# Kernel tuning notes

Hardware: AMD Instinct MI355X
Metric: run time of the kernel (lower is better)

## Reference

```python
import jax, jax.numpy as jnp
import numpy as np

GRAPH_ALPHA = 3.0
HOP_ALPHA = 0.05
TOP_K = 30


def conv1x1(x, W, b):
    # x: [B,C,N,T], W: [O,C] -> [B,O,N,T]
    return jnp.einsum('bcnt,oc->bont', x, W) + b[None, :, None, None]


def tconv(x, W, b):
    # temporal conv along T, kernel (1,3), 'same' padding. W: [O,I,1,3]
    y = jax.lax.conv_general_dilated(x, W, (1, 1), ((0, 0), (1, 1)),
                                     dimension_numbers=('NCHW', 'OIHW', 'NCHW'))
    return y + b[None, :, None, None]


def mixprop(x, adj, W, b):
    # 1-hop mix-prop graph diffusion (gcn_depth=1, hopalpha=0.05)
    n = adj.shape[0]
    A = adj + jnp.eye(n, dtype=adj.dtype)
    A = A / A.sum(axis=1, keepdims=True)
    h = HOP_ALPHA * x + (1.0 - HOP_ALPHA) * jnp.einsum('bcvt,vw->bcwt', x, A)
    return conv1x1(jnp.concatenate([x, h], axis=1), W, b)


def st_block(x, adj, tf_w, tf_b, tg_w, tg_b, g1_w, g1_b, g2_w, g2_b,
             end_w, end_b, out_w, out_b):
    h = jnp.tanh(tconv(x, tf_w, tf_b)) * jax.nn.sigmoid(tconv(x, tg_w, tg_b))
    h = mixprop(h, adj, g1_w, g1_b) + mixprop(h, adj.T, g2_w, g2_b)
    h = jax.nn.relu(conv1x1(h, end_w, end_b))
    return conv1x1(h, out_w, out_b)


def build_adj(idx, emb1, emb2, l1_w, l1_b, l2_w, l2_b):
    e1, e2 = emb1[idx], emb2[idx]
    n1 = jnp.tanh(GRAPH_ALPHA * (e1 @ l1_w.T + l1_b))
    n2 = jnp.tanh(GRAPH_ALPHA * (e2 @ l2_w.T + l2_b))
    a = n1 @ n2.T - n2 @ n1.T
    adj = jax.nn.relu(jnp.tanh(GRAPH_ALPHA * a))
    _, top_idx = jax.lax.top_k(adj, TOP_K)
    rows = jnp.arange(adj.shape[0])[:, None]
    mask = jnp.zeros_like(adj).at[rows, top_idx].set(1.0)
    return adj * mask


def setup_inputs() -> dict:
    B, T, N, D = 16, 128, 1024, 64
    ks = jax.random.split(jax.random.key(0), 24)
    def w(i, shape):
        return jax.random.normal(ks[i], shape, dtype=jnp.float32) * 0.1
    z = lambda *s: jnp.zeros(s, jnp.float32)
    return {
        'x': jax.random.normal(ks[0], (B, T, N), dtype=jnp.float32),
        'idx': jnp.arange(N, dtype=jnp.int32),
        'emb1': w(1, (N, D)), 'emb2': w(2, (N, D)),
        'lin1_w': w(3, (D, D)), 'lin1_b': z(D),
        'lin2_w': w(4, (D, D)), 'lin2_b': z(D),
        'w_start': w(5, (16, 1)), 'b_start': z(16),
        'enc_tf_w': w(6, (16, 16, 1, 3)), 'enc_tf_b': z(16),
        'enc_tg_w': w(7, (16, 16, 1, 3)), 'enc_tg_b': z(16),
        'enc_g1_w': w(8, (16, 32)), 'enc_g1_b': z(16),
        'enc_g2_w': w(9, (16, 32)), 'enc_g2_b': z(16),
        'enc_end_w': w(10, (32, 16)), 'enc_end_b': z(32),
        'enc_out_w': w(11, (64, 32)), 'enc_out_b': z(64),
        'dec_tf_w': w(12, (64, 64, 1, 3)), 'dec_tf_b': z(64),
        'dec_tg_w': w(13, (64, 64, 1, 3)), 'dec_tg_b': z(64),
        'dec_g1_w': w(14, (64, 128)), 'dec_g1_b': z(64),
        'dec_g2_w': w(15, (64, 128)), 'dec_g2_b': z(64),
        'dec_end_w': w(16, (32, 64)), 'dec_end_b': z(32),
        'dec_out_w': w(17, (16, 32)), 'dec_out_b': z(16),
        'w_end': w(18, (1, 16)), 'b_end': z(1),
    }


def reference(x, idx, emb1, emb2, lin1_w, lin1_b, lin2_w, lin2_b,
              w_start, b_start,
              enc_tf_w, enc_tf_b, enc_tg_w, enc_tg_b, enc_g1_w, enc_g1_b,
              enc_g2_w, enc_g2_b, enc_end_w, enc_end_b, enc_out_w, enc_out_b,
              dec_tf_w, dec_tf_b, dec_tg_w, dec_tg_b, dec_g1_w, dec_g1_b,
              dec_g2_w, dec_g2_b, dec_end_w, dec_end_b, dec_out_w, dec_out_b,
              w_end, b_end):
    adj = build_adj(idx, emb1, emb2, lin1_w, lin1_b, lin2_w, lin2_b)
    h = jnp.transpose(x, (0, 2, 1))[:, None]  # [B,1,N,T]
    h = conv1x1(h, w_start, b_start)          # [B,16,N,T]
    z = st_block(h, adj, enc_tf_w, enc_tf_b, enc_tg_w, enc_tg_b,
                 enc_g1_w, enc_g1_b, enc_g2_w, enc_g2_b,
                 enc_end_w, enc_end_b, enc_out_w, enc_out_b)  # [B,64,N,T]
    y = st_block(z, adj, dec_tf_w, dec_tf_b, dec_tg_w, dec_tg_b,
                 dec_g1_w, dec_g1_b, dec_g2_w, dec_g2_b,
                 dec_end_w, dec_end_b, dec_out_w, dec_out_b)  # [B,16,N,T]
    y = conv1x1(y, w_end, b_end)               # [B,1,N,T]
    return jnp.transpose(y[:, 0], (0, 2, 1))   # [B,T,N]
```

## Files before the change

kernel.cpp:

```cpp
#include <hip/hip_runtime.h>
#include <math.h>

#define NN   1024
#define TTL  128
#define NTP  131072
#define TOPK 30

#define OEGTF_T 0
#define OEGTF_C 48
#define OEGTF_B 96
#define OEGTG_T 112
#define OEGTG_C 160
#define OEGTG_B 208
#define OEE0    224
#define OEE1    736
#define OEE2    1248
#define OEEB    1760
#define OEOUT_W 1792
#define OEOUT_B 3840
#define ODTF_B  16192
#define ODTG_B  28544
#define ODEB    34752
#define OWC     34784
#define OBC     34816
#define ODEALL  59456
#define ODTW2   65600
#define OCF     77888
#define OCG     78080
#define WTOT    78272


__global__ void k_prep_weights(
    const float* __restrict__ w_start, const float* __restrict__ b_start,
    const float* __restrict__ etf_w, const float* __restrict__ etf_b,
    const float* __restrict__ etg_w, const float* __restrict__ etg_b,
    const float* __restrict__ eg1_w, const float* __restrict__ eg1_b,
    const float* __restrict__ eg2_w, const float* __restrict__ eg2_b,
    const float* __restrict__ eend_w, const float* __restrict__ eend_b,
    const float* __restrict__ eout_w, const float* __restrict__ eout_b,
    const float* __restrict__ dtf_w, const float* __restrict__ dtf_b,
    const float* __restrict__ dtg_w, const float* __restrict__ dtg_b,
    const float* __restrict__ dg1_w, const float* __restrict__ dg1_b,
    const float* __restrict__ dg2_w, const float* __restrict__ dg2_b,
    const float* __restrict__ dend_w, const float* __restrict__ dend_b,
    const float* __restrict__ dout_w, const float* __restrict__ dout_b,
    const float* __restrict__ w_end, const float* __restrict__ b_end,
    float* __restrict__ W)
{
    int tid = blockIdx.x*blockDim.x + threadIdx.x;
    int nthr = gridDim.x*blockDim.x;
    for (int id=tid; id<96; id+=nthr){
        int which = id/48; int r = id%48; int o = r/3, k = r%3;
        const float* w = which ? etg_w : etf_w;
        double t=0.0, c=0.0;
        for (int i=0;i<16;i++){
            double wv = (double)w[(o*16+i)*3+k];
            t += wv*(double)w_start[i];
            c += wv*(double)b_start[i];
        }
        W[(which?OEGTG_T:OEGTF_T)+o*3+k] = (float)t;
        W[(which?OEGTG_C:OEGTF_C)+o*3+k] = (float)c;
    }
    for (int i=tid;i<16;i+=nthr){
        W[OEGTF_B+i] = etf_b[i];
        W[OEGTG_B+i] = etg_b[i];
    }
    for (int id=tid; id<512; id+=nthr){
        int i = id>>5, o2 = id&31;
        double s0=0.0, s1=0.0, s2=0.0;
        for (int o=0;o<16;o++){
            double m0 = (double)eg1_w[o*32+i] + (double)eg2_w[o*32+i]
                      + 0.05*((double)eg1_w[o*32+16+i] + (double)eg2_w[o*32+16+i]);
            double m1 = 0.95*(double)eg1_w[o*32+16+i];
            double m2 = 0.95*(double)eg2_w[o*32+16+i];
            double ew = (double)eend_w[o2*16+o];
            s0 += ew*m0; s1 += ew*m1; s2 += ew*m2;
        }
        W[OEE0+i*32+o2]=(float)s0; W[OEE1+i*32+o2]=(float)s1; W[OEE2+i*32+o2]=(float)s2;
    }
    for (int o2=tid; o2<32; o2+=nthr){
        double s = (double)eend_b[o2];
        for (int o=0;o<16;o++) s += (double)eend_w[o2*16+o]*((double)eg1_b[o]+(double)eg2_b[o]);
        W[OEEB+o2] = (float)s;
    }
    for (int i=tid;i<64;i+=nthr){
        W[ODTF_B+i]=dtf_b[i]; W[ODTG_B+i]=dtg_b[i];
    }
    for (int id=tid; id<12288; id+=nthr){
        int oc = id/3072; int rem = id%3072; int j = rem/96; int q = rem%96;
        const float* w = (q<48) ? dtf_w : dtg_w;
        int q2 = (q<48) ? q : q-48;
        int o = q2/3, k = q2%3;
        double s = 0.0;
        for (int i=0;i<64;i++)
            s += (double)w[((oc*16+o)*64+i)*3+k]*(double)eout_w[i*32+j];
        W[ODTW2+id] = (float)s;
    }
    for (int id=tid; id<384; id+=nthr){
        int which = id/192; int r = id%192;
        int oc = r/48; int q = r%48; int o = q/3, k = q%3;
        const float* w = which ? dtg_w : dtf_w;
        double s = 0.0;
        for (int i=0;i<64;i++)
            s += (double)w[((oc*16+o)*64+i)*3+k]*(double)eout_b[i];
        W[(which?OCG:OCF) + oc*48 + o*3 + k] = (float)s;
    }
    for (int id=tid; id<6144; id+=nthr){
        int i = id/96, j = id%96;
        double s = 0.0;
        if (j < 32){
            int o2 = j;
            for (int o=0;o<64;o++){
                double m1 = 0.95*(double)dg1_w[o*128+64+i];
                s += (double)dend_w[o2*64+o]*m1;
            }
        } else if (j < 64){
            int o2 = j-32;
            for (int o=0;o<64;o++){
                double m2 = 0.95*(double)dg2_w[o*128+64+i];
                s += (double)dend_w[o2*64+o]*m2;
            }
        } else {
            int o2 = j-64;
            for (int o=0;o<64;o++){
                double m0 = (double)dg1_w[o*128+i] + (double)dg2_w[o*128+i]
                          + 0.05*((double)dg1_w[o*128+64+i] + (double)dg2_w[o*128+64+i]);
                s += (double)dend_w[o2*64+o]*m0;
            }
        }
        W[ODEALL+id] = (float)s;
    }
    for (int o2=tid; o2<32; o2+=nthr){
        double s = (double)dend_b[o2];
        for (int o=0;o<64;o++) s += (double)dend_w[o2*64+o]*((double)dg1_b[o]+(double)dg2_b[o]);
        W[ODEB+o2] = (float)s;
        double wc = 0.0;
        for (int o3=0;o3<16;o3++) wc += (double)w_end[o3]*(double)dout_w[o3*32+o2];
        W[OWC+o2] = (float)wc;
    }
    if (tid==0){
        double bc = (double)b_end[0];
        for (int o3=0;o3<16;o3++) bc += (double)w_end[o3]*(double)dout_b[o3];
        W[OBC] = (float)bc;
    }
}

__global__ void k_emb(const int* __restrict__ idxp,
                      const float* __restrict__ emb1, const float* __restrict__ emb2,
                      const float* __restrict__ l1w, const float* __restrict__ l1b,
                      const float* __restrict__ l2w, const float* __restrict__ l2b,
                      double* __restrict__ n1, double* __restrict__ n2)
{
    int id = blockIdx.x*blockDim.x + threadIdx.x;
    int i = id>>6, d = id&63;
    int ii = idxp[i];
    double a1 = (double)l1b[d], a2 = (double)l2b[d];
    for (int k=0;k<64;k++){
        a1 += (double)emb1[ii*64+k]*(double)l1w[d*64+k];
        a2 += (double)emb2[ii*64+k]*(double)l2w[d*64+k];
    }
    n1[id] = tanh(3.0*a1);
    n2[id] = tanh(3.0*a2);
}

__global__ __launch_bounds__(256) void k_topk(
    const double* __restrict__ n1, const double* __restrict__ n2,
    int* __restrict__ topc, double* __restrict__ topv,
    double* __restrict__ rs1, double* __restrict__ colsum)
{
    __shared__ double arow[NN];
    __shared__ double sn1[64], sn2[64];
    __shared__ double rvs[4];
    __shared__ int    rjs[4];
    int i = blockIdx.x, tid = threadIdx.x;
    int lane = tid & 63, wid = tid >> 6;
    if (tid < 64){ sn1[tid] = n1[i*64+tid]; sn2[tid] = n2[i*64+tid]; }
    __syncthreads();
    for (int jb=0;jb<4;jb++){
        int j = jb*256 + tid;
        const double* p2 = n2 + (long)j*64;
        const double* p1 = n1 + (long)j*64;
        double d1v=0.0, d2v=0.0;
        for (int d=0;d<64;d++){ d1v += sn1[d]*p2[d]; d2v += sn2[d]*p1[d]; }
        double a = tanh(3.0*(d1v - d2v));
        arow[j] = a>0.0 ? a : 0.0;
    }
    __syncthreads();
    double rsum = 0.0;
    for (int r=0;r<TOPK;r++){
        double bv = -2.0; int bj = 1<<30;
        #pragma unroll
        for (int jb=0;jb<4;jb++){
            int j = jb*256+tid;
            double v = arow[j];
            if (v>bv || (v==bv && j<bj)){ bv=v; bj=j; }
        }
        for (int off=32; off>=1; off>>=1){
            double ov = __shfl_xor(bv, off, 64);
            int    oj = __shfl_xor(bj, off, 64);
            if (ov>bv || (ov==bv && oj<bj)){ bv=ov; bj=oj; }
        }
        if (lane == 0){ rvs[wid]=bv; rjs[wid]=bj; }
        __syncthreads();
        bv = rvs[0]; bj = rjs[0];
        #pragma unroll
        for (int k2=1;k2<4;k2++){
            double ov = rvs[k2]; int oj = rjs[k2];
            if (ov>bv || (ov==bv && oj<bj)){ bv=ov; bj=oj; }
        }
        if (tid == (bj & 255)) arow[bj] = -2.0;
        if (tid == 0){
            topc[i*TOPK+r] = bj;
            topv[i*TOPK+r] = bv;
            if (bv > 0.0) atomicAdd(&colsum[bj], bv);
        }
        rsum += (bv > 0.0 ? bv : 0.0);
        __syncthreads();
    }
    if (tid == 0) rs1[i] = 1.0 + rsum;
}

__global__ void k_csc(const int* __restrict__ topc, const double* __restrict__ topv,
                      const double* __restrict__ rs1,
                      int* __restrict__ ccount, int* __restrict__ cidx, float* __restrict__ cw)
{
    int w = blockIdx.x*blockDim.x + threadIdx.x;
    if (w >= NN) return;
    double rv = rs1[w];
    for (int r=0;r<TOPK;r++){
        double v = topv[w*TOPK+r];
        if (v > 0.0){
            int col = topc[w*TOPK+r];
            int pos = atomicAdd(&ccount[col], 1);
            cidx[(long)col*NN+pos] = w;
            cw  [(long)col*NN+pos] = (float)(v / rv);
        }
    }
}

__global__ void k_pad(int* __restrict__ ccount, int* __restrict__ cidx, float* __restrict__ cw)
{
    int col = blockIdx.x*blockDim.x + threadIdx.x;
    if (col >= NN) return;
    int cnt = ccount[col];
    int padded = (cnt + 7) & ~7;
    for (int e = cnt; e < padded; e++){
        cidx[(long)col*NN + e] = 0;
        cw  [(long)col*NN + e] = 0.0f;
    }
    ccount[col] = padded;
}

__global__ void k_post1(const double* __restrict__ colsum, const double* __restrict__ rs1,
                        double* __restrict__ rs2, float* __restrict__ d1, float* __restrict__ d2)
{
    int v = blockIdx.x*blockDim.x + threadIdx.x;
    if (v >= NN) return;
    double r2 = 1.0 + colsum[v];
    rs2[v] = r2;
    d2[v] = (float)(1.0/r2);
    d1[v] = (float)(1.0/rs1[v]);
}

__global__ void k_post2(const int* __restrict__ topc, const double* __restrict__ topv,
                        const double* __restrict__ rs2,
                        int* __restrict__ topc2, float* __restrict__ ew2b)
{
    int e = blockIdx.x*blockDim.x + threadIdx.x;
    if (e >= NN*32) return;
    int w = e>>5, r = e&31;
    if (r < TOPK){
        double v = topv[w*TOPK+r];
        int c = topc[w*TOPK+r];
        topc2[e] = (v > 0.0) ? c : 0;
        ew2b[e]  = (v > 0.0) ? (float)(v / rs2[c]) : 0.0f;
    } else {
        topc2[e] = 0;
        ew2b[e]  = 0.0f;
    }
}


__global__ __launch_bounds__(256) void k_enc_gg(const float* __restrict__ x,
    float* __restrict__ eg, float* __restrict__ es1, float* __restrict__ es2,
    const float* __restrict__ Wt,
    const int* __restrict__ ccount, const int* __restrict__ cidx, const float* __restrict__ cw,
    const int* __restrict__ topc2, const float* __restrict__ ew2b,
    const float* __restrict__ d1, const float* __restrict__ d2,
    long S, int b0)
{
    __shared__ float4 lds4[NN];
    int tid = threadIdx.x, c = blockIdx.y, cb = blockIdx.z, t0 = blockIdx.x*4;
    float ft[3], fc[3], gt[3], gcc[3];
    #pragma unroll
    for (int k=0;k<3;k++){
        ft[k]=Wt[OEGTF_T+c*3+k]; fc[k]=Wt[OEGTF_C+c*3+k];
        gt[k]=Wt[OEGTG_T+c*3+k]; gcc[k]=Wt[OEGTG_C+c*3+k];
    }
    float fb = Wt[OEGTF_B+c], gb = Wt[OEGTG_B+c];
    const float* xb = x + (long)(b0+cb)*NTP + (long)t0*NN;
    long base = (long)c*S + (long)cb*NTP + (long)t0*NN;
    bool hl0 = (t0>0), hr3 = (t0+4<TTL);
    for (int q=0;q<4;q++){
        int v = q*256 + tid;
        float xm = hl0 ? xb[v-NN] : 0.0f;
        float x0 = xb[v], x1 = xb[v+NN], x2 = xb[v+2*NN], x3 = xb[v+3*NN];
        float xq = hr3 ? xb[v+4*NN] : 0.0f;
        float g0,g1,g2,g3;
        {
            float atf = fb + ft[1]*x0 + fc[1], atg = gb + gt[1]*x0 + gcc[1];
            if (hl0){ atf += ft[0]*xm + fc[0]; atg += gt[0]*xm + gcc[0]; }
            atf += ft[2]*x1 + fc[2]; atg += gt[2]*x1 + gcc[2];
            g0 = tanhf(atf)/(1.0f+expf(-atg));
        }
        {
            float atf = fb + ft[0]*x0 + fc[0] + ft[1]*x1 + fc[1] + ft[2]*x2 + fc[2];
            float atg = gb + gt[0]*x0 + gcc[0] + gt[1]*x1 + gcc[1] + gt[2]*x2 + gcc[2];
            g1 = tanhf(atf)/(1.0f+expf(-atg));
        }
        {
            float atf = fb + ft[0]*x1 + fc[0] + ft[1]*x2 + fc[1] + ft[2]*x3 + fc[2];
            float atg = gb + gt[0]*x1 + gcc[0] + gt[1]*x2 + gcc[1] + gt[2]*x3 + gcc[2];
            g2 = tanhf(atf)/(1.0f+expf(-atg));
        }
        {
            float atf = fb + ft[0]*x2 + fc[0] + ft[1]*x3 + fc[1];
            float atg = gb + gt[0]*x2 + gcc[0] + gt[1]*x3 + gcc[1];
            if (hr3){ atf += ft[2]*xq + fc[2]; atg += gt[2]*xq + gcc[2]; }
            g3 = tanhf(atf)/(1.0f+expf(-atg));
        }
        lds4[v] = make_float4(g0,g1,g2,g3);
        eg[base+v] = g0; eg[base+NN+v] = g1; eg[base+2*NN+v] = g2; eg[base+3*NN+v] = g3;
    }
    __syncthreads();
    for (int wb=0;wb<4;wb++){
        int w = wb*256 + tid;
        float4 gw = lds4[w];
        float dv = d1[w];
        float a0=gw.x*dv, a1=gw.y*dv, a2=gw.z*dv, a3=gw.w*dv;
        int cnt = ccount[w];
        const int4*   ci4 = (const int4*)  (cidx + (long)w*NN);
        const float4* cw4 = (const float4*)(cw   + (long)w*NN);
        for (int e=0; e<cnt; e+=8){
            int4 ia = ci4[e>>2], ib = ci4[(e>>2)+1];
            float4 wa = cw4[e>>2], wc = cw4[(e>>2)+1];
            float4 s;
            s = lds4[ia.x]; a0 += wa.x*s.x; a1 += wa.x*s.y; a2 += wa.x*s.z; a3 += wa.x*s.w;
            s = lds4[ia.y]; a0 += wa.y*s.x; a1 += wa.y*s.y; a2 += wa.y*s.z; a3 += wa.y*s.w;
            s = lds4[ia.z]; a0 += wa.z*s.x; a1 += wa.z*s.y; a2 += wa.z*s.z; a3 += wa.z*s.w;
            s = lds4[ia.w]; a0 += wa.w*s.x; a1 += wa.w*s.y; a2 += wa.w*s.z; a3 += wa.w*s.w;
            s = lds4[ib.x]; a0 += wc.x*s.x; a1 += wc.x*s.y; a2 += wc.x*s.z; a3 += wc.x*s.w;
            s = lds4[ib.y]; a0 += wc.y*s.x; a1 += wc.y*s.y; a2 += wc.y*s.z; a3 += wc.y*s.w;
            s = lds4[ib.z]; a0 += wc.z*s.x; a1 += wc.z*s.y; a2 += wc.z*s.z; a3 += wc.z*s.w;
            s = lds4[ib.w]; a0 += wc.w*s.x; a1 += wc.w*s.y; a2 += wc.w*s.z; a3 += wc.w*s.w;
        }
        es1[base+w]=a0; es1[base+NN+w]=a1; es1[base+2*NN+w]=a2; es1[base+3*NN+w]=a3;
        float dw = d2[w];
        float b0a=gw.x*dw, b1a=gw.y*dw, b2a=gw.z*dw, b3a=gw.w*dw;
        const int4*   tc4 = (const int4*)  (topc2 + w*32);
        const float4* e24 = (const float4*)(ew2b  + w*32);
        #pragma unroll
        for (int r=0;r<8;r++){
            int4 ic = tc4[r]; float4 wv = e24[r];
            float4 s;
            s = lds4[ic.x]; b0a += wv.x*s.x; b1a += wv.x*s.y; b2a += wv.x*s.z; b3a += wv.x*s.w;
            s = lds4[ic.y]; b0a += wv.y*s.x; b1a += wv.y*s.y; b2a += wv.y*s.z; b3a += wv.y*s.w;
            s = lds4[ic.z]; b0a += wv.z*s.x; b1a += wv.z*s.y; b2a += wv.z*s.z; b3a += wv.z*s.w;
            s = lds4[ic.w]; b0a += wv.w*s.x; b1a += wv.w*s.y; b2a += wv.w*s.z; b3a += wv.w*s.w;
        }
        es2[base+w]=b0a; es2[base+NN+w]=b1a; es2[base+2*NN+w]=b2a; es2[base+3*NN+w]=b3a;
    }
}

__global__ __launch_bounds__(256) void k_enc_tail(const float* __restrict__ Bp,
    float* __restrict__ E32, const float* __restrict__ Wt, long S)
{
    long p = (long)blockIdx.x*256 + threadIdx.x;
    float e[32];
    #pragma unroll
    for (int o2=0;o2<32;o2++) e[o2] = Wt[OEEB+o2];
    for (int i=0;i<16;i++){
        float a = Bp[(long)i*S+p], b = Bp[(long)(16+i)*S+p], c = Bp[(long)(32+i)*S+p];
        const float* w0 = Wt+OEE0+i*32;
        const float* w1 = Wt+OEE1+i*32;
        const float* w2 = Wt+OEE2+i*32;
        #pragma unroll
        for (int o2=0;o2<32;o2++) e[o2] += w0[o2]*a + w1[o2]*b + w2[o2]*c;
    }
    #pragma unroll
    for (int o2=0;o2<32;o2++){
        float v = e[o2];
        E32[(long)o2*S+p] = v>0.0f ? v : 0.0f;
    }
}

__global__ __launch_bounds__(256) void k_dec_gate(const float* __restrict__ E32,
    float* __restrict__ g, const float* __restrict__ Wt, long S)
{
    int oc = blockIdx.y, cb = blockIdx.z;
    int bx = blockIdx.x;
    int vseg = bx & 3, tpair = bx >> 2;
    int t0 = tpair*2;
    long pos0 = (long)cb*NTP + (long)t0*NN + vseg*256 + threadIdx.x;
    bool hasL = (t0 > 0), hasR = (t0 + 2 < TTL);
    float af0[16], ag0[16], af1[16], ag1[16];
    const float* CFo = Wt + OCF + oc*48;
    const float* CGo = Wt + OCG + oc*48;
    #pragma unroll
    for (int o=0;o<16;o++){
        float fB = Wt[ODTF_B+oc*16+o], gB = Wt[ODTG_B+oc*16+o];
        float f0 = CFo[o*3], f1 = CFo[o*3+1], f2 = CFo[o*3+2];
        float h0 = CGo[o*3], h1 = CGo[o*3+1], h2 = CGo[o*3+2];
        af0[o] = fB + f1 + f2 + (hasL ? f0 : 0.0f);
        ag0[o] = gB + h1 + h2 + (hasL ? h0 : 0.0f);
        af1[o] = fB + f0 + f1 + (hasR ? f2 : 0.0f);
        ag1[o] = gB + h0 + h1 + (hasR ? h2 : 0.0f);
    }
    #pragma unroll 2
    for (int j=0;j<32;j++){
        const float* xp = E32 + (long)j*S + pos0;
        float xl0 = hasL ? xp[-NN] : 0.0f;
        float xc0 = xp[0];
        float xc1 = xp[NN];
        float xr1 = hasR ? xp[2*NN] : 0.0f;
        const float* wfg = Wt + ODTW2 + (long)(oc*32+j)*96;
        #pragma unroll
        for (int o=0;o<16;o++){
            float w0=wfg[o*3], w1=wfg[o*3+1], w2=wfg[o*3+2];
            af0[o] += w0*xl0 + w1*xc0 + w2*xc1;
            af1[o] += w0*xc0 + w1*xc1 + w2*xr1;
            float v0=wfg[48+o*3], v1=wfg[48+o*3+1], v2=wfg[48+o*3+2];
            ag0[o] += v0*xl0 + v1*xc0 + v2*xc1;
            ag1[o] += v0*xc0 + v1*xc1 + v2*xr1;
        }
    }
    #pragma unroll
    for (int o=0;o<16;o++){
        long op = (long)(oc*16+o)*S + pos0;
        g[op]    = tanhf(af0[o])/(1.0f+expf(-ag0[o]));
        g[op+NN] = tanhf(af1[o])/(1.0f+expf(-ag1[o]));
    }
}

__global__ __launch_bounds__(256) void k_dec_conv(const float* __restrict__ g,
    float* __restrict__ P12, float* __restrict__ P0p,
    const float* __restrict__ Wt, long S)
{
    long p = (long)blockIdx.x*256 + threadIdx.x;
    float a0[32], a1[32], a2[32];
    #pragma unroll
    for (int jj=0;jj<32;jj++){ a1[jj]=0.0f; a2[jj]=0.0f; a0[jj]=Wt[ODEB+jj]; }
    #pragma unroll 1
    for (int i=0;i<64;i++){
        float gv = g[(long)i*S+p];
        const float* wr = Wt + ODEALL + i*96;
        #pragma unroll
        for (int jj=0;jj<32;jj++){
            a1[jj] += wr[jj]*gv;
            a2[jj] += wr[32+jj]*gv;
            a0[jj] += wr[64+jj]*gv;
        }
    }
    #pragma unroll
    for (int jj=0;jj<32;jj++){
        P12[(long)jj*S+p]      = a1[jj];
        P12[(long)(32+jj)*S+p] = a2[jj];
        P0p[(long)jj*S+p]      = a0[jj];
    }
}

__global__ __launch_bounds__(256) void k_graph32f(const float* __restrict__ P1,
    const float* __restrict__ P2, const float* __restrict__ P0,
    float* __restrict__ part,
    const int* __restrict__ ccount, const int* __restrict__ cidx, const float* __restrict__ cw,
    const int* __restrict__ topc2, const float* __restrict__ ew2b,
    const float* __restrict__ d1, const float* __restrict__ d2,
    const float* __restrict__ Wt, long S)
{
    __shared__ float4 lds4[NN];
    int tid = threadIdx.x;
    int grp = blockIdx.y, cb = blockIdx.z, t0 = blockIdx.x*4;
    long tbase = (long)cb*NTP + (long)t0*NN;
    float res[4][4];
    #pragma unroll
    for (int wb=0;wb<4;wb++){
        #pragma unroll
        for (int k=0;k<4;k++) res[wb][k]=0.0f;
    }
    float q1[4][4];
    for (int c4=0;c4<4;c4++){
        int ch = grp*4 + c4;
        long base = (long)ch*S + tbase;
        if (c4) __syncthreads();
        const float* s1 = P1 + base;
        for (int q=0;q<4;q++){
            int v = q*256 + tid;
            lds4[v] = make_float4(s1[v], s1[v+NN], s1[v+2*NN], s1[v+3*NN]);
        }
        __syncthreads();
        for (int wb=0;wb<4;wb++){
            int w = wb*256 + tid;
            float4 gv = lds4[w];
            float dv = d1[w];
            float a0=gv.x*dv, a1=gv.y*dv, a2=gv.z*dv, a3=gv.w*dv;
            int cnt = ccount[w];
            const int4*   ci4 = (const int4*)  (cidx + (long)w*NN);
            const float4* cw4 = (const float4*)(cw   + (long)w*NN);
            for (int e=0; e<cnt; e+=8){
                int4 ia = ci4[e>>2], ib = ci4[(e>>2)+1];
                float4 wa = cw4[e>>2], wc2 = cw4[(e>>2)+1];
                float4 s;
                s = lds4[ia.x]; a0 += wa.x*s.x; a1 += wa.x*s.y; a2 += wa.x*s.z; a3 += wa.x*s.w;
                s = lds4[ia.y]; a0 += wa.y*s.x; a1 += wa.y*s.y; a2 += wa.y*s.z; a3 += wa.y*s.w;
                s = lds4[ia.z]; a0 += wa.z*s.x; a1 += wa.z*s.y; a2 += wa.z*s.z; a3 += wa.z*s.w;
                s = lds4[ia.w]; a0 += wa.w*s.x; a1 += wa.w*s.y; a2 += wa.w*s.z; a3 += wa.w*s.w;
                s = lds4[ib.x]; a0 += wc2.x*s.x; a1 += wc2.x*s.y; a2 += wc2.x*s.z; a3 += wc2.x*s.w;
                s = lds4[ib.y]; a0 += wc2.y*s.x; a1 += wc2.y*s.y; a2 += wc2.y*s.z; a3 += wc2.y*s.w;
                s = lds4[ib.z]; a0 += wc2.z*s.x; a1 += wc2.z*s.y; a2 += wc2.z*s.z; a3 += wc2.z*s.w;
                s = lds4[ib.w]; a0 += wc2.w*s.x; a1 += wc2.w*s.y; a2 += wc2.w*s.z; a3 += wc2.w*s.w;
            }
            q1[wb][0]=a0; q1[wb][1]=a1; q1[wb][2]=a2; q1[wb][3]=a3;
        }
        __syncthreads();
        const float* s2 = P2 + base;
        for (int q=0;q<4;q++){
            int v = q*256 + tid;
            lds4[v] = make_float4(s2[v], s2[v+NN], s2[v+2*NN], s2[v+3*NN]);
        }
        __syncthreads();
        float wc = Wt[OWC+ch];
        const float* p0 = P0 + base;
        for (int wb=0;wb<4;wb++){
            int w = wb*256 + tid;
            float4 gv = lds4[w];
            float dw = d2[w];
            float c0=gv.x*dw, c1=gv.y*dw, c2=gv.z*dw, c3=gv.w*dw;
            const int4*   tc4 = (const int4*)  (topc2 + w*32);
            const float4* e24 = (const float4*)(ew2b  + w*32);
            #pragma unroll
            for (int r=0;r<8;r++){
                int4 ic = tc4[r]; float4 wv = e24[r];
                float4 s;
                s = lds4[ic.x]; c0 += wv.x*s.x; c1 += wv.x*s.y; c2 += wv.x*s.z; c3 += wv.x*s.w;
                s = lds4[ic.y]; c0 += wv.y*s.x; c1 += wv.y*s.y; c2 += wv.y*s.z; c3 += wv.y*s.w;
                s = lds4[ic.z]; c0 += wv.z*s.x; c1 += wv.z*s.y; c2 += wv.z*s.z; c3 += wv.z*s.w;
                s = lds4[ic.w]; c0 += wv.w*s.x; c1 += wv.w*s.y; c2 += wv.w*s.z; c3 += wv.w*s.w;
            }
            float e0 = p0[w]        + q1[wb][0] + c0;
            float e1 = p0[NN+w]     + q1[wb][1] + c1;
            float e2 = p0[2*NN+w]   + q1[wb][2] + c2;
            float e3 = p0[3*NN+w]   + q1[wb][3] + c3;
            e0 = e0>0.0f?e0:0.0f; e1 = e1>0.0f?e1:0.0f;
            e2 = e2>0.0f?e2:0.0f; e3 = e3>0.0f?e3:0.0f;
            res[wb][0] += wc*e0; res[wb][1] += wc*e1;
            res[wb][2] += wc*e2; res[wb][3] += wc*e3;
        }
    }
    long pb = (long)grp*S + tbase;
    for (int wb=0;wb<4;wb++){
        int w = wb*256 + tid;
        part[pb+w]      = res[wb][0];
        part[pb+NN+w]   = res[wb][1];
        part[pb+2*NN+w] = res[wb][2];
        part[pb+3*NN+w] = res[wb][3];
    }
}

__global__ __launch_bounds__(256) void k_comb(const float* __restrict__ part,
    const float* __restrict__ Wt, float* __restrict__ out, long S, int b0)
{
    long p = (long)blockIdx.x*256 + threadIdx.x;
    float r = Wt[OBC];
    #pragma unroll
    for (int gp=0; gp<8; gp++) r += part[(long)gp*S+p];
    out[(long)b0*NTP + p] = r;
}


extern "C" void kernel_launch(void* const* d_in, const int* in_sizes, int n_in,
                              void* d_out, int out_size, void* d_ws, size_t ws_size,
                              hipStream_t stream)
{
    const float* x      = (const float*)d_in[0];
    const int*   idx    = (const int*)  d_in[1];
    const float* emb1   = (const float*)d_in[2];
    const float* emb2   = (const float*)d_in[3];
    const float* lin1_w = (const float*)d_in[4];
    const float* lin1_b = (const float*)d_in[5];
    const float* lin2_w = (const float*)d_in[6];
    const float* lin2_b = (const float*)d_in[7];
    const float* w_start= (const float*)d_in[8];
    const float* b_start= (const float*)d_in[9];
    const float* etf_w  = (const float*)d_in[10];
    const float* etf_b  = (const float*)d_in[11];
    const float* etg_w  = (const float*)d_in[12];
    const float* etg_b  = (const float*)d_in[13];
    const float* eg1_w  = (const float*)d_in[14];
    const float* eg1_b  = (const float*)d_in[15];
    const float* eg2_w  = (const float*)d_in[16];
    const float* eg2_b  = (const float*)d_in[17];
    const float* eend_w = (const float*)d_in[18];
    const float* eend_b = (const float*)d_in[19];
    const float* eout_w = (const float*)d_in[20];
    const float* eout_b = (const float*)d_in[21];
    const float* dtf_w  = (const float*)d_in[22];
    const float* dtf_b  = (const float*)d_in[23];
    const float* dtg_w  = (const float*)d_in[24];
    const float* dtg_b  = (const float*)d_in[25];
    const float* dg1_w  = (const float*)d_in[26];
    const float* dg1_b  = (const float*)d_in[27];
    const float* dg2_w  = (const float*)d_in[28];
    const float* dg2_b  = (const float*)d_in[29];
    const float* dend_w = (const float*)d_in[30];
    const float* dend_b = (const float*)d_in[31];
    const float* dout_w = (const float*)d_in[32];
    const float* dout_b = (const float*)d_in[33];
    const float* w_end  = (const float*)d_in[34];
    const float* b_end  = (const float*)d_in[35];
    float* out = (float*)d_out;

    char* basep = (char*)d_ws;
    size_t cur = 0;
    auto alloc = [&](size_t bytes)->void* {
        void* p = basep + cur;
        cur = (cur + bytes + 511) & ~(size_t)511;
        return p;
    };
    float*  W     = (float*) alloc(WTOT*sizeof(float));
    double* n1    = (double*)alloc(65536*sizeof(double));
    double* n2    = (double*)alloc(65536*sizeof(double));
    double* topv  = (double*)alloc((size_t)NN*TOPK*sizeof(double));
    int*    topc  = (int*)   alloc((size_t)NN*TOPK*sizeof(int));
    double* rs1   = (double*)alloc(NN*sizeof(double));
    double* rs2   = (double*)alloc(NN*sizeof(double));
    double* colsum= (double*)alloc(NN*sizeof(double));
    float*  d1a   = (float*) alloc(NN*sizeof(float));
    float*  d2a   = (float*) alloc(NN*sizeof(float));
    int*    topc2 = (int*)   alloc((size_t)NN*32*sizeof(int));
    float*  ew2b  = (float*) alloc((size_t)NN*32*sizeof(float));
    int*    ccount= (int*)   alloc(NN*sizeof(int));
    int*    cidx  = (int*)   alloc((size_t)NN*NN*sizeof(int));
    float*  cw    = (float*) alloc((size_t)NN*NN*sizeof(float));

    size_t perb = (size_t)176 * NTP * sizeof(float);
    int CB = 1;
    for (int c = 16; c >= 1; c >>= 1){
        if (cur + perb*(size_t)c <= ws_size){ CB = c; break; }
    }
    long S = (long)CB * NTP;
    float* A = (float*)alloc((size_t)64*S*sizeof(float));
    float* B = (float*)alloc((size_t)48*S*sizeof(float));
    float* C = (float*)alloc((size_t)64*S*sizeof(float));

    (void)hipMemsetAsync(colsum, 0, NN*sizeof(double), stream);
    (void)hipMemsetAsync(ccount, 0, NN*sizeof(int), stream);

    k_prep_weights<<<32,256,0,stream>>>(
        w_start,b_start, etf_w,etf_b, etg_w,etg_b, eg1_w,eg1_b, eg2_w,eg2_b,
        eend_w,eend_b, eout_w,eout_b, dtf_w,dtf_b, dtg_w,dtg_b, dg1_w,dg1_b,
        dg2_w,dg2_b, dend_w,dend_b, dout_w,dout_b, w_end,b_end, W);
    k_emb<<<256,256,0,stream>>>(idx, emb1, emb2, lin1_w, lin1_b, lin2_w, lin2_b, n1, n2);
    k_topk<<<NN,256,0,stream>>>(n1, n2, topc, topv, rs1, colsum);
    k_csc<<<4,256,0,stream>>>(topc, topv, rs1, ccount, cidx, cw);
    k_pad<<<4,256,0,stream>>>(ccount, cidx, cw);
    k_post1<<<4,256,0,stream>>>(colsum, rs1, rs2, d1a, d2a);
    k_post2<<<(NN*32+255)/256,256,0,stream>>>(topc, topv, rs2, topc2, ew2b);

    int nch = 16 / CB;
    for (int ch=0; ch<nch; ch++){
        int b0 = ch*CB;
        k_enc_gg<<<dim3(32,16,CB),256,0,stream>>>(x, B, B+(long)16*S, B+(long)32*S, W,
            ccount,cidx,cw, topc2,ew2b, d1a,d2a, S, b0);
        k_enc_tail<<<512*CB,256,0,stream>>>(B, A, W, S);
        k_dec_gate<<<dim3(256,4,CB),256,0,stream>>>(A, C, W, S);
        k_dec_conv<<<512*CB,256,0,stream>>>(C, A, B, W, S);
        k_graph32f<<<dim3(32,8,CB),256,0,stream>>>(A, A+(long)32*S, B, C,
            ccount,cidx,cw, topc2,ew2b, d1a,d2a, W, S);
        k_comb<<<512*CB,256,0,stream>>>(C, W, out, S, b0);
    }
    (void)in_sizes; (void)n_in; (void)out_size;
}
```

Baseline: 4.010 ms.

## Use single-wavefront top-k with incremental rescans and one timestep per thread in dec_gate

The top-k kernel now runs as a single 64-lane wavefront per row. It keeps a per-lane running maximum, and after each selection only the lane that owned the winner rescans its 16 entries, which removes the block-wide barriers and the full rescan every round. The decoder gate kernel drops the two-timesteps-per-thread blocking in favour of one timestep per thread over a flattened grid. That halves the accumulator registers but loses the reuse of the shared centre and neighbour loads and weight reads across adjacent timesteps, so the gate kernel may do more memory and weight-load work per output.

```diff
diff --git a/kernel.cpp b/kernel.cpp
--- a/kernel.cpp
+++ b/kernel.cpp
@@ -163,21 +163,19 @@
     n2[id] = tanh(3.0*a2);
 }
 
-__global__ __launch_bounds__(256) void k_topk(
+__global__ __launch_bounds__(64) void k_topk(
     const double* __restrict__ n1, const double* __restrict__ n2,
     int* __restrict__ topc, double* __restrict__ topv,
     double* __restrict__ rs1, double* __restrict__ colsum)
 {
     __shared__ double arow[NN];
     __shared__ double sn1[64], sn2[64];
-    __shared__ double rvs[4];
-    __shared__ int    rjs[4];
-    int i = blockIdx.x, tid = threadIdx.x;
-    int lane = tid & 63, wid = tid >> 6;
-    if (tid < 64){ sn1[tid] = n1[i*64+tid]; sn2[tid] = n2[i*64+tid]; }
+    int i = blockIdx.x, lane = threadIdx.x;
+    sn1[lane] = n1[i*64+lane];
+    sn2[lane] = n2[i*64+lane];
     __syncthreads();
-    for (int jb=0;jb<4;jb++){
-        int j = jb*256 + tid;
+    for (int jb=0;jb<16;jb++){
+        int j = jb*64 + lane;
         const double* p2 = n2 + (long)j*64;
         const double* p1 = n1 + (long)j*64;
         double d1v=0.0, d2v=0.0;
@@ -186,38 +184,37 @@
         arow[j] = a>0.0 ? a : 0.0;
     }
     __syncthreads();
+    double lv = -2.0; int lj = 1<<30;
+    for (int jb=0;jb<16;jb++){
+        int j = jb*64+lane;
+        double v = arow[j];
+        if (v>lv || (v==lv && j<lj)){ lv=v; lj=j; }
+    }
     double rsum = 0.0;
     for (int r=0;r<TOPK;r++){
-        double bv = -2.0; int bj = 1<<30;
-        #pragma unroll
-        for (int jb=0;jb<4;jb++){
-            int j = jb*256+tid;
-            double v = arow[j];
-            if (v>bv || (v==bv && j<bj)){ bv=v; bj=j; }
-        }
+        double bv = lv; int bj = lj;
         for (int off=32; off>=1; off>>=1){
             double ov = __shfl_xor(bv, off, 64);
             int    oj = __shfl_xor(bj, off, 64);
             if (ov>bv || (ov==bv && oj<bj)){ bv=ov; bj=oj; }
         }
-        if (lane == 0){ rvs[wid]=bv; rjs[wid]=bj; }
-        __syncthreads();
-        bv = rvs[0]; bj = rjs[0];
-        #pragma unroll
-        for (int k2=1;k2<4;k2++){
-            double ov = rvs[k2]; int oj = rjs[k2];
-            if (ov>bv || (ov==bv && oj<bj)){ bv=ov; bj=oj; }
-        }
-        if (tid == (bj & 255)) arow[bj] = -2.0;
-        if (tid == 0){
+        if (lane == (bj & 63)){
+            arow[bj] = -2.0;
+            lv = -2.0; lj = 1<<30;
+            for (int jb=0;jb<16;jb++){
+                int j = jb*64+lane;
+                double v = arow[j];
+                if (v>lv || (v==lv && j<lj)){ lv=v; lj=j; }
+            }
+        }
+        if (lane == 0){
             topc[i*TOPK+r] = bj;
             topv[i*TOPK+r] = bv;
             if (bv > 0.0) atomicAdd(&colsum[bj], bv);
         }
         rsum += (bv > 0.0 ? bv : 0.0);
-        __syncthreads();
-    }
-    if (tid == 0) rs1[i] = 1.0 + rsum;
+    }
+    if (lane == 0) rs1[i] = 1.0 + rsum;
 }
 
 __global__ void k_csc(const int* __restrict__ topc, const double* __restrict__ topv,
@@ -397,48 +394,35 @@
 __global__ __launch_bounds__(256) void k_dec_gate(const float* __restrict__ E32,
     float* __restrict__ g, const float* __restrict__ Wt, long S)
 {
-    int oc = blockIdx.y, cb = blockIdx.z;
-    int bx = blockIdx.x;
-    int vseg = bx & 3, tpair = bx >> 2;
-    int t0 = tpair*2;
-    long pos0 = (long)cb*NTP + (long)t0*NN + vseg*256 + threadIdx.x;
-    bool hasL = (t0 > 0), hasR = (t0 + 2 < TTL);
-    float af0[16], ag0[16], af1[16], ag1[16];
-    const float* CFo = Wt + OCF + oc*48;
-    const float* CGo = Wt + OCG + oc*48;
+    int oc = blockIdx.y;
+    long pos = (long)blockIdx.x*256 + threadIdx.x;
+    int t = (int)((pos>>10) & (TTL-1));
+    bool hasL = (t>0), hasR = (t<TTL-1);
+    float af[16], ag[16];
     #pragma unroll
     for (int o=0;o<16;o++){
-        float fB = Wt[ODTF_B+oc*16+o], gB = Wt[ODTG_B+oc*16+o];
-        float f0 = CFo[o*3], f1 = CFo[o*3+1], f2 = CFo[o*3+2];
-        float h0 = CGo[o*3], h1 = CGo[o*3+1], h2 = CGo[o*3+2];
-        af0[o] = fB + f1 + f2 + (hasL ? f0 : 0.0f);
-        ag0[o] = gB + h1 + h2 + (hasL ? h0 : 0.0f);
-        af1[o] = fB + f0 + f1 + (hasR ? f2 : 0.0f);
-        ag1[o] = gB + h0 + h1 + (hasR ? h2 : 0.0f);
-    }
-    #pragma unroll 2
+        float bf = Wt[ODTF_B+oc*16+o] + Wt[OCF+oc*48+o*3+1];
+        float bg = Wt[ODTG_B+oc*16+o] + Wt[OCG+oc*48+o*3+1];
+        if (hasL){ bf += Wt[OCF+oc*48+o*3];   bg += Wt[OCG+oc*48+o*3]; }
+        if (hasR){ bf += Wt[OCF+oc*48+o*3+2]; bg += Wt[OCG+oc*48+o*3+2]; }
+        af[o]=bf; ag[o]=bg;
+    }
+    #pragma unroll 1
     for (int j=0;j<32;j++){
-        const float* xp = E32 + (long)j*S + pos0;
-        float xl0 = hasL ? xp[-NN] : 0.0f;
-        float xc0 = xp[0];
-        float xc1 = xp[NN];
-        float xr1 = hasR ? xp[2*NN] : 0.0f;
+        const float* xp = E32 + (long)j*S + pos;
+        float xc = xp[0];
+        float xl = hasL ? xp[-NN] : 0.0f;
+        float xr = hasR ? xp[NN]  : 0.0f;
         const float* wfg = Wt + ODTW2 + (long)(oc*32+j)*96;
         #pragma unroll
         for (int o=0;o<16;o++){
-            float w0=wfg[o*3], w1=wfg[o*3+1], w2=wfg[o*3+2];
-            af0[o] += w0*xl0 + w1*xc0 + w2*xc1;
-            af1[o] += w0*xc0 + w1*xc1 + w2*xr1;
-            float v0=wfg[48+o*3], v1=wfg[48+o*3+1], v2=wfg[48+o*3+2];
-            ag0[o] += v0*xl0 + v1*xc0 + v2*xc1;
-            ag1[o] += v0*xc0 + v1*xc1 + v2*xr1;
+            af[o] += wfg[o*3]*xl + wfg[o*3+1]*xc + wfg[o*3+2]*xr;
+            ag[o] += wfg[48+o*3]*xl + wfg[48+o*3+1]*xc + wfg[48+o*3+2]*xr;
         }
     }
     #pragma unroll
     for (int o=0;o<16;o++){
-        long op = (long)(oc*16+o)*S + pos0;
-        g[op]    = tanhf(af0[o])/(1.0f+expf(-ag0[o]));
-        g[op+NN] = tanhf(af1[o])/(1.0f+expf(-ag1[o]));
+        g[(long)(oc*16+o)*S + pos] = tanhf(af[o])/(1.0f+expf(-ag[o]));
     }
 }
 
@@ -660,7 +644,7 @@
         eend_w,eend_b, eout_w,eout_b, dtf_w,dtf_b, dtg_w,dtg_b, dg1_w,dg1_b,
         dg2_w,dg2_b, dend_w,dend_b, dout_w,dout_b, w_end,b_end, W);
     k_emb<<<256,256,0,stream>>>(idx, emb1, emb2, lin1_w, lin1_b, lin2_w, lin2_b, n1, n2);
-    k_topk<<<NN,256,0,stream>>>(n1, n2, topc, topv, rs1, colsum);
+    k_topk<<<NN,64,0,stream>>>(n1, n2, topc, topv, rs1, colsum);
     k_csc<<<4,256,0,stream>>>(topc, topv, rs1, ccount, cidx, cw);
     k_pad<<<4,256,0,stream>>>(ccount, cidx, cw);
     k_post1<<<4,256,0,stream>>>(colsum, rs1, rs2, d1a, d2a);
@@ -672,7 +656,7 @@
         k_enc_gg<<<dim3(32,16,CB),256,0,stream>>>(x, B, B+(long)16*S, B+(long)32*S, W,
             ccount,cidx,cw, topc2,ew2b, d1a,d2a, S, b0);
         k_enc_tail<<<512*CB,256,0,stream>>>(B, A, W, S);
-        k_dec_gate<<<dim3(256,4,CB),256,0,stream>>>(A, C, W, S);
+        k_dec_gate<<<dim3(512*CB,4),256,0,stream>>>(A, C, W, S);
         k_dec_conv<<<512*CB,256,0,stream>>>(C, A, B, W, S);
         k_graph32f<<<dim3(32,8,CB),256,0,stream>>>(A, A+(long)32*S, B, C,
             ccount,cidx,cw, topc2,ew2b, d1a,d2a, W, S);
```

After: 3.952 ms. Within noise of the previous version (-1.4%).
